# Optimization experiments

Hardware: AMD Instinct MI355X
Metric: run time of the kernel (lower is better)

## Reference

```python
import jax, jax.numpy as jnp
import numpy as np

N_QUBITS = 12
N_LAYERS = 3


def _apply_1q(state, U, q):
    # state: (2,)*N_QUBITS complex64, U: (2,2) single-qubit gate on wire q
    r = jnp.tensordot(U, state, axes=([1], [q]))
    return jnp.moveaxis(r, 0, q)


def _apply_cnot(state, c, t):
    M = jnp.array([[1, 0, 0, 0], [0, 1, 0, 0], [0, 0, 0, 1], [0, 0, 1, 0]],
                  jnp.complex64).reshape(2, 2, 2, 2)
    r = jnp.tensordot(M, state, axes=([2, 3], [c, t]))
    return jnp.moveaxis(r, (0, 1), (c, t))


def circuit_expvals(weights):
    # weights: (N_LAYERS, N_QUBITS, 3). Circuit starts from |0...0> (the
    # TorchLayer 'inputs' arg is a dummy and unused in the original qnode).
    state = jnp.zeros((2,) * N_QUBITS, jnp.complex64).at[(0,) * N_QUBITS].set(1.0)
    zero = jnp.zeros((), jnp.complex64)
    for l in range(N_LAYERS):
        for q in range(N_QUBITS):
            tx, ty, tz = weights[l, q, 0], weights[l, q, 1], weights[l, q, 2]
            cx = jnp.cos(tx / 2).astype(jnp.complex64)
            sx = jnp.sin(tx / 2).astype(jnp.complex64)
            RX = jnp.stack([jnp.stack([cx, -1j * sx]), jnp.stack([-1j * sx, cx])])
            cy = jnp.cos(ty / 2).astype(jnp.complex64)
            sy = jnp.sin(ty / 2).astype(jnp.complex64)
            RY = jnp.stack([jnp.stack([cy, -sy]), jnp.stack([sy, cy])])
            tzc = tz.astype(jnp.complex64)
            em, ep = jnp.exp(-1j * tzc / 2), jnp.exp(1j * tzc / 2)
            RZ = jnp.stack([jnp.stack([em, zero]), jnp.stack([zero, ep])])
            # RX then RY then RZ applied to the state => matrix RZ @ RY @ RX
            state = _apply_1q(state, RZ @ RY @ RX, q)
        for q in range(N_QUBITS):
            state = _apply_cnot(state, q, (q + 1) % N_QUBITS)
    probs = state.real ** 2 + state.imag ** 2
    exps = []
    for q in range(N_QUBITS):
        marg = probs.sum(axis=tuple(a for a in range(N_QUBITS) if a != q))  # (2,)
        exps.append(marg[0] - marg[1])  # <Z_q>
    return jnp.stack(exps).astype(jnp.float32)  # (12,)


def setup_inputs() -> dict:
    key = jax.random.key(0)
    ks = jax.random.split(key, 5)
    B = 1048576
    images = jax.random.uniform(ks[0], (B, 1, 4, 4), dtype=jnp.float32)
    qweights = jax.random.normal(ks[1], (N_LAYERS, N_QUBITS, 3), dtype=jnp.float32)
    W1 = jax.random.normal(ks[2], (32, 12), dtype=jnp.float32) * (1.0 / np.sqrt(12))
    b1 = jnp.zeros((32,), jnp.float32)
    W2 = jax.random.normal(ks[3], (16, 32), dtype=jnp.float32) * (1.0 / np.sqrt(32))
    b2 = jnp.zeros((16,), jnp.float32)
    return {"images": images, "qweights": qweights, "W1": W1, "b1": b1,
            "W2": W2, "b2": b2}


def reference(images, qweights, W1, b1, W2, b2):
    # The original forward ignores the amplitude-encoded image state and runs
    # the identical circuit (dummy zero input) for every batch element, so the
    # per-sample result is constant across the batch.
    z = circuit_expvals(qweights)                     # (12,)
    h = jax.nn.relu(z @ W1.T + b1)                    # (32,)
    pix = jax.nn.sigmoid(h @ W2.T + b2)               # (16,)
    B = images.shape[0]
    return jnp.broadcast_to(pix.reshape(1, 1, 4, 4), (B, 1, 4, 4))
```

## Files before the change

kernel.cpp:

```cpp
#include <hip/hip_runtime.h>
#include <math.h>

#define NTH 512

typedef float v4f __attribute__((ext_vector_type(4)));

__device__ __forceinline__ int Sw(int i) { return i ^ ((i >> 6) & 7); }

__device__ __forceinline__ int Fr(int i) {
    int x = i; x ^= x >> 1; x ^= x >> 2; x ^= x >> 4; x ^= x >> 8;
    return (x & 0x7FF) | (((x ^ (i >> 11)) & 1) << 11);
}

__device__ __forceinline__ float2 cmul(float2 a, float2 b) {
    return make_float2(a.x*b.x - a.y*b.y, a.x*b.y + a.y*b.x);
}

__device__ __forceinline__ void apply2(const float4 u0, const float4 u1,
                                       float2& v0, float2& v1) {
    const float n0r = u0.x*v0.x - u0.y*v0.y + u0.z*v1.x - u0.w*v1.y;
    const float n0i = u0.x*v0.y + u0.y*v0.x + u0.z*v1.y + u0.w*v1.x;
    const float n1r = u1.x*v0.x - u1.y*v0.y + u1.z*v1.x - u1.w*v1.y;
    const float n1i = u1.x*v0.y + u1.y*v0.x + u1.z*v1.y + u1.w*v1.x;
    v0 = make_float2(n0r, n0i);
    v1 = make_float2(n1r, n1i);
}

template<int PLOW, int MODE>
__device__ __forceinline__ void do_pass(float2* amp, const float4 (*gmat)[2],
                                        int gbase, int t, float* zacc) {
    int base;
    if      (PLOW == 9) base = t;
    else if (PLOW == 6) base = ((t >> 6) << 9) | (t & 63);
    else if (PLOW == 3) base = ((t >> 3) << 6) | (t & 7);
    else                base = t << 3;

    float2 v[8]; int idx[8];
    #pragma unroll
    for (int r = 0; r < 8; ++r) {
        idx[r] = Sw(base | (r << PLOW));
        v[r] = amp[idx[r]];
    }
    #pragma unroll
    for (int k = 2; k >= 0; --k) {
        const int q = 11 - (PLOW + k);
        const float4 u0 = gmat[gbase + q][0];
        const float4 u1 = gmat[gbase + q][1];
        const int m = 1 << k;
        #pragma unroll
        for (int r = 0; r < 8; ++r)
            if (!(r & m)) apply2(u0, u1, v[r], v[r | m]);
    }
    if (MODE == 0) {
        #pragma unroll
        for (int r = 0; r < 8; ++r) amp[idx[r]] = v[r];
    } else if (MODE == 1) {
        __syncthreads();
        #pragma unroll
        for (int r = 0; r < 8; ++r) amp[Sw(Fr(base | (r << PLOW)))] = v[r];
    } else {
        #pragma unroll
        for (int r = 0; r < 8; ++r) {
            const int x = Fr(base | (r << PLOW));
            const float p = v[r].x*v[r].x + v[r].y*v[r].y;
            #pragma unroll
            for (int q = 0; q < 12; ++q)
                zacc[q] += ((x >> (11 - q)) & 1) ? -p : p;
        }
    }
}

__global__ __launch_bounds__(NTH) void circuit_kernel(
    const float* __restrict__ qw,
    const float* __restrict__ W1,
    const float* __restrict__ b1,
    const float* __restrict__ W2,
    const float* __restrict__ b2,
    float* __restrict__ pix)
{
    __shared__ float2 amp[4096];
    __shared__ float4 gmat[36][2];
    __shared__ float  zp2[96];

    const int tid  = threadIdx.x;
    const int lane = tid & 63;
    const int wv   = tid >> 6;

    float W1row[12], W2row[32], b1v = 0.f, b2v = 0.f;
    #pragma unroll
    for (int k = 0; k < 12; ++k) W1row[k] = 0.f;
    #pragma unroll
    for (int k = 0; k < 32; ++k) W2row[k] = 0.f;
    if (tid < 32) {
        b1v = b1[tid];
        #pragma unroll
        for (int k = 0; k < 12; ++k) W1row[k] = W1[tid*12 + k];
    }
    if (tid < 16) {
        b2v = b2[tid];
        #pragma unroll
        for (int k = 0; k < 32; ++k) W2row[k] = W2[tid*32 + k];
    }

    if (tid < 36) {
        float sx, cx, sy, cy, sz, cz;
        sincosf(0.5f * qw[tid*3+0], &sx, &cx);
        sincosf(0.5f * qw[tid*3+1], &sy, &cy);
        sincosf(0.5f * qw[tid*3+2], &sz, &cz);
        const float a00r =  cy*cx, a00i =  sy*sx;
        const float a01r = -sy*cx, a01i = -cy*sx;
        const float a10r =  sy*cx, a10i = -cy*sx;
        const float a11r =  cy*cx, a11i = -sy*sx;
        gmat[tid][0] = make_float4(cz*a00r + sz*a00i, cz*a00i - sz*a00r,
                                   cz*a01r + sz*a01i, cz*a01i - sz*a01r);
        gmat[tid][1] = make_float4(cz*a10r - sz*a10i, cz*a10i + sz*a10r,
                                   cz*a11r - sz*a11i, cz*a11i + sz*a11r);
    }
    __syncthreads();

    {
        float2 pp = make_float2(1.f, 0.f);
        #pragma unroll
        for (int b = 11; b >= 3; --b) {
            const int q = 11 - b;
            const float4 g = gmat[q][(tid >> (b - 3)) & 1];
            pp = cmul(pp, make_float2(g.x, g.y));
        }
        float2 c9[2], c10[2], c11[2];
        #pragma unroll
        for (int s = 0; s < 2; ++s) {
            c9[s]  = make_float2(gmat[9][s].x,  gmat[9][s].y);
            c10[s] = make_float2(gmat[10][s].x, gmat[10][s].y);
            c11[s] = make_float2(gmat[11][s].x, gmat[11][s].y);
        }
        #pragma unroll
        for (int r = 0; r < 8; ++r) {
            const float2 v = cmul(pp,
                cmul(c9[(r>>2)&1], cmul(c10[(r>>1)&1], c11[r&1])));
            amp[Sw(Fr((tid << 3) | r))] = v;
        }
    }
    __syncthreads();

    float zacc[12];
    #pragma unroll
    for (int q = 0; q < 12; ++q) zacc[q] = 0.f;

    do_pass<9,0>(amp, gmat, 12, tid, zacc); __syncthreads();
    do_pass<6,0>(amp, gmat, 12, tid, zacc); __syncthreads();
    do_pass<3,0>(amp, gmat, 12, tid, zacc); __syncthreads();
    do_pass<0,1>(amp, gmat, 12, tid, zacc); __syncthreads();
    do_pass<9,0>(amp, gmat, 24, tid, zacc); __syncthreads();
    do_pass<6,0>(amp, gmat, 24, tid, zacc); __syncthreads();
    do_pass<3,0>(amp, gmat, 24, tid, zacc); __syncthreads();
    do_pass<0,2>(amp, gmat, 24, tid, zacc);

    float z6[6];
    #pragma unroll
    for (int k = 0; k < 6; ++k) {
        const float send = (lane & 1) ? zacc[k]   : zacc[k+6];
        const float keep = (lane & 1) ? zacc[k+6] : zacc[k];
        z6[k] = keep + __shfl_xor(send, 1);
    }
    float z3[3];
    #pragma unroll
    for (int k = 0; k < 3; ++k) {
        const float send = (lane & 2) ? z6[k]   : z6[k+3];
        const float keep = (lane & 2) ? z6[k+3] : z6[k];
        z3[k] = keep + __shfl_xor(send, 2);
    }
    #pragma unroll
    for (int m = 4; m <= 32; m <<= 1) {
        #pragma unroll
        for (int k = 0; k < 3; ++k) z3[k] += __shfl_xor(z3[k], m);
    }
    if (lane < 4) {
        const int qb = 6*(lane & 1) + 3*((lane >> 1) & 1);
        #pragma unroll
        for (int k = 0; k < 3; ++k) zp2[wv*12 + qb + k] = z3[k];
    }
    __syncthreads();

    if (tid < 64) {
        float s = 0.f;
        if (tid < 12) {
            #pragma unroll
            for (int w8 = 0; w8 < 8; ++w8) s += zp2[w8*12 + tid];
        }
        float acc = b1v;
        #pragma unroll
        for (int k = 0; k < 12; ++k) acc += W1row[k] * __shfl(s, k);
        const float h = acc > 0.f ? acc : 0.f;
        float acc2 = b2v;
        #pragma unroll
        for (int k = 0; k < 32; ++k) acc2 += W2row[k] * __shfl(h, k);
        if (tid < 16) pix[tid] = 1.f / (1.f + expf(-acc2));
    }
}

__global__ __launch_bounds__(256) void bcast_kernel(
    const v4f* __restrict__ pix4, v4f* __restrict__ out4)
{
    const int i = blockIdx.x * 256 + threadIdx.x;
    const v4f val = pix4[i & 3];
    __builtin_nontemporal_store(val, &out4[i]);
}

extern "C" void kernel_launch(void* const* d_in, const int* in_sizes, int n_in,
                              void* d_out, int out_size, void* d_ws, size_t ws_size,
                              hipStream_t stream) {
    const float* qw = (const float*)d_in[1];
    const float* W1 = (const float*)d_in[2];
    const float* b1 = (const float*)d_in[3];
    const float* W2 = (const float*)d_in[4];
    const float* b2 = (const float*)d_in[5];
    float* pix = (float*)d_ws;

    circuit_kernel<<<1, NTH, 0, stream>>>(qw, W1, b1, W2, b2, pix);

    const int n4 = out_size / 4;
    bcast_kernel<<<n4 / 256, 256, 0, stream>>>((const v4f*)pix,
                                               (v4f*)d_out);
}
```

Baseline: 123.6 us.

## Process 16 amplitudes per thread with 256 threads and double-buffered LDS

The circuit kernel now runs 256 threads, each holding 16 amplitudes, so each layer needs three radix-16 passes instead of four radix-8 passes, cutting the number of barriers and LDS round trips. The XOR swizzle is replaced by padding (i + i>>4), and a second buffer is used for the CNOT permutation pass, so the extra mid-pass __syncthreads is no longer needed. This trades fewer threads and more registers per thread for fewer synchronisations. The total runtime is likely dominated by the 16 MB broadcast kernel, which is unchanged.

```diff
diff --git a/kernel.cpp b/kernel.cpp
--- a/kernel.cpp
+++ b/kernel.cpp
@@ -1,11 +1,11 @@
 #include <hip/hip_runtime.h>
 #include <math.h>
 
-#define NTH 512
+#define NTH 256
 
 typedef float v4f __attribute__((ext_vector_type(4)));
 
-__device__ __forceinline__ int Sw(int i) { return i ^ ((i >> 6) & 7); }
+__device__ __forceinline__ int Ph(int i) { return i + (i >> 4); }
 
 __device__ __forceinline__ int Fr(int i) {
     int x = i; x ^= x >> 1; x ^= x >> 2; x ^= x >> 4; x ^= x >> 8;
@@ -26,46 +26,42 @@
     v1 = make_float2(n1r, n1i);
 }
 
-template<int PLOW, int MODE>
-__device__ __forceinline__ void do_pass(float2* amp, const float4 (*gmat)[2],
-                                        int gbase, int t, float* zacc) {
+template<int SH, int MODE>
+__device__ __forceinline__ void do_pass16(const float2* __restrict__ src,
+                                          float2* __restrict__ dst,
+                                          const float4 (*gmat)[2],
+                                          int gbase, int t, float* zacc) {
     int base;
-    if      (PLOW == 9) base = t;
-    else if (PLOW == 6) base = ((t >> 6) << 9) | (t & 63);
-    else if (PLOW == 3) base = ((t >> 3) << 6) | (t & 7);
-    else                base = t << 3;
-
-    float2 v[8]; int idx[8];
-    #pragma unroll
-    for (int r = 0; r < 8; ++r) {
-        idx[r] = Sw(base | (r << PLOW));
-        v[r] = amp[idx[r]];
-    }
-    #pragma unroll
-    for (int k = 2; k >= 0; --k) {
-        const int q = 11 - (PLOW + k);
+    if      (SH == 0) base = t << 4;
+    else if (SH == 4) base = ((t >> 4) << 8) | (t & 15);
+    else              base = t;
+
+    float2 v[16];
+    #pragma unroll
+    for (int r = 0; r < 16; ++r) v[r] = src[Ph(base | (r << SH))];
+    #pragma unroll
+    for (int k = 3; k >= 0; --k) {
+        const int q = 11 - (SH + k);
         const float4 u0 = gmat[gbase + q][0];
         const float4 u1 = gmat[gbase + q][1];
-        const int m = 1 << k;
-        #pragma unroll
-        for (int r = 0; r < 8; ++r)
-            if (!(r & m)) apply2(u0, u1, v[r], v[r | m]);
+        #pragma unroll
+        for (int r = 0; r < 16; ++r)
+            if (!(r & (1 << k))) apply2(u0, u1, v[r], v[r | (1 << k)]);
     }
     if (MODE == 0) {
         #pragma unroll
-        for (int r = 0; r < 8; ++r) amp[idx[r]] = v[r];
+        for (int r = 0; r < 16; ++r) dst[Ph(base | (r << SH))] = v[r];
     } else if (MODE == 1) {
-        __syncthreads();
-        #pragma unroll
-        for (int r = 0; r < 8; ++r) amp[Sw(Fr(base | (r << PLOW)))] = v[r];
+        #pragma unroll
+        for (int r = 0; r < 16; ++r) dst[Ph(Fr(base | (r << SH)))] = v[r];
     } else {
         #pragma unroll
-        for (int r = 0; r < 8; ++r) {
-            const int x = Fr(base | (r << PLOW));
+        for (int r = 0; r < 16; ++r) {
+            const int x = Fr(base | (r << SH));
             const float p = v[r].x*v[r].x + v[r].y*v[r].y;
             #pragma unroll
-            for (int q = 0; q < 12; ++q)
-                zacc[q] += ((x >> (11 - q)) & 1) ? -p : p;
+            for (int q2 = 0; q2 < 12; ++q2)
+                zacc[q2] += ((x >> (11 - q2)) & 1) ? -p : p;
         }
     }
 }
@@ -78,9 +74,10 @@
     const float* __restrict__ b2,
     float* __restrict__ pix)
 {
-    __shared__ float2 amp[4096];
+    __shared__ float2 ampA[4352];
+    __shared__ float2 ampB[4352];
     __shared__ float4 gmat[36][2];
-    __shared__ float  zp2[96];
+    __shared__ float  zp2[48];
 
     const int tid  = threadIdx.x;
     const int lane = tid & 63;
@@ -121,23 +118,29 @@
     {
         float2 pp = make_float2(1.f, 0.f);
         #pragma unroll
-        for (int b = 11; b >= 3; --b) {
+        for (int b = 11; b >= 4; --b) {
             const int q = 11 - b;
-            const float4 g = gmat[q][(tid >> (b - 3)) & 1];
+            const float4 g = gmat[q][(tid >> (b - 4)) & 1];
             pp = cmul(pp, make_float2(g.x, g.y));
         }
-        float2 c9[2], c10[2], c11[2];
+        float2 c8[2], c9[2], c10[2], c11[2];
         #pragma unroll
         for (int s = 0; s < 2; ++s) {
+            c8[s]  = make_float2(gmat[8][s].x,  gmat[8][s].y);
             c9[s]  = make_float2(gmat[9][s].x,  gmat[9][s].y);
             c10[s] = make_float2(gmat[10][s].x, gmat[10][s].y);
             c11[s] = make_float2(gmat[11][s].x, gmat[11][s].y);
         }
-        #pragma unroll
-        for (int r = 0; r < 8; ++r) {
-            const float2 v = cmul(pp,
-                cmul(c9[(r>>2)&1], cmul(c10[(r>>1)&1], c11[r&1])));
-            amp[Sw(Fr((tid << 3) | r))] = v;
+        float2 hi[4], lo[4];
+        #pragma unroll
+        for (int s = 0; s < 4; ++s) {
+            hi[s] = cmul(c8[(s >> 1) & 1],  c9[s & 1]);
+            lo[s] = cmul(c10[(s >> 1) & 1], c11[s & 1]);
+        }
+        #pragma unroll
+        for (int r = 0; r < 16; ++r) {
+            const float2 v = cmul(pp, cmul(hi[r >> 2], lo[r & 3]));
+            ampA[Ph(Fr((tid << 4) | r))] = v;
         }
     }
     __syncthreads();
@@ -146,14 +149,12 @@
     #pragma unroll
     for (int q = 0; q < 12; ++q) zacc[q] = 0.f;
 
-    do_pass<9,0>(amp, gmat, 12, tid, zacc); __syncthreads();
-    do_pass<6,0>(amp, gmat, 12, tid, zacc); __syncthreads();
-    do_pass<3,0>(amp, gmat, 12, tid, zacc); __syncthreads();
-    do_pass<0,1>(amp, gmat, 12, tid, zacc); __syncthreads();
-    do_pass<9,0>(amp, gmat, 24, tid, zacc); __syncthreads();
-    do_pass<6,0>(amp, gmat, 24, tid, zacc); __syncthreads();
-    do_pass<3,0>(amp, gmat, 24, tid, zacc); __syncthreads();
-    do_pass<0,2>(amp, gmat, 24, tid, zacc);
+    do_pass16<0,0>(ampA, ampA, gmat, 12, tid, zacc); __syncthreads();
+    do_pass16<4,0>(ampA, ampA, gmat, 12, tid, zacc); __syncthreads();
+    do_pass16<8,1>(ampA, ampB, gmat, 12, tid, zacc); __syncthreads();
+    do_pass16<0,0>(ampB, ampB, gmat, 24, tid, zacc); __syncthreads();
+    do_pass16<4,0>(ampB, ampB, gmat, 24, tid, zacc); __syncthreads();
+    do_pass16<8,2>(ampB, ampB, gmat, 24, tid, zacc);
 
     float z6[6];
     #pragma unroll
@@ -185,7 +186,7 @@
         float s = 0.f;
         if (tid < 12) {
             #pragma unroll
-            for (int w8 = 0; w8 < 8; ++w8) s += zp2[w8*12 + tid];
+            for (int w4 = 0; w4 < 4; ++w4) s += zp2[w4*12 + tid];
         }
         float acc = b1v;
         #pragma unroll
```

Result: slower. 127.6 us (+3.2%).
